# Optimization experiments

Measured on AMD Instinct MI355X. Metric: run time of the kernel, lower is better.

Reference implementation:

```python
import jax, jax.numpy as jnp
import numpy as np

N_NODES = 50000
N_EDGES = 600000
IN_CH, HID1, HID2, OUT_CH = 128, 256, 128, 2


def setup_inputs() -> dict:
    key = jax.random.key(0)
    ks = jax.random.split(key, 8)
    x = jax.random.normal(ks[0], (N_NODES, IN_CH), dtype=jnp.float32)
    edge_index = jax.random.randint(ks[1], (2, N_EDGES), 0, N_NODES, dtype=jnp.int64)
    # Glorot-style init for GCN linear weights
    def glorot(k, fan_in, fan_out):
        s = jnp.sqrt(6.0 / (fan_in + fan_out)).astype(jnp.float32)
        return jax.random.uniform(k, (fan_in, fan_out), jnp.float32, -s, s)
    return {
        "x": x,
        "W1": glorot(ks[2], IN_CH, HID1), "b1": jnp.zeros((HID1,), jnp.float32),
        "W2": glorot(ks[3], HID1, HID2), "b2": jnp.zeros((HID2,), jnp.float32),
        "W3": glorot(ks[4], HID2, OUT_CH), "b3": jnp.zeros((OUT_CH,), jnp.float32),
        "edge_index": edge_index,
    }


def _gcn_graph(edge_index, n_nodes):
    # Add self-loops (GCNConv default) and compute symmetric normalization
    loop = jnp.arange(n_nodes, dtype=edge_index.dtype)
    src = jnp.concatenate([edge_index[0], loop])
    dst = jnp.concatenate([edge_index[1], loop])
    ones = jnp.ones(src.shape[0], dtype=jnp.float32)
    deg = jax.ops.segment_sum(ones, dst, num_segments=n_nodes)
    dinv = jnp.where(deg > 0, jax.lax.rsqrt(deg), 0.0)
    norm = dinv[src] * dinv[dst]  # [E + N]
    return src, dst, norm


def _gcn_layer(h, W, b, src, dst, norm, n_nodes):
    h = h @ W                                   # [N, d_out]
    msg = h[src] * norm[:, None]                # gather + scale  [E+N, d_out]
    agg = jax.ops.segment_sum(msg, dst, num_segments=n_nodes)
    return agg + b


def reference(x, W1, b1, W2, b2, W3, b3, edge_index):
    n = x.shape[0]
    src, dst, norm = _gcn_graph(edge_index, n)
    h = jax.nn.relu(_gcn_layer(x, W1, b1, src, dst, norm, n))
    # dropout p=0.5 is identity in eval mode (training=False)
    h = jax.nn.relu(_gcn_layer(h, W2, b2, src, dst, norm, n))
    h = _gcn_layer(h, W3, b3, src, dst, norm, n)
    return jax.nn.log_softmax(h, axis=1)
```

## Files before the change

kernel.cpp:

```cpp
#include <hip/hip_runtime.h>
#include <hip/hip_bf16.h>
#include <math.h>

#define N_NODES 50000
#define N_EDGES 600000
#define E_TOT   (N_EDGES + N_NODES)
#define M_PAD   50048
#define NODE_STRIDE 32
#define DUMMY_ROWS 65536
#define CSR_CAP (N_NODES * NODE_STRIDE + 2048)

typedef __attribute__((ext_vector_type(8))) short bf16x8;
typedef __attribute__((ext_vector_type(4))) float f32x4;
typedef __attribute__((ext_vector_type(2))) float f32x2;
typedef __attribute__((ext_vector_type(8))) unsigned short u16x8;


__device__ __forceinline__ unsigned short f2bf(float f) {
    unsigned int u = __float_as_uint(f);
    unsigned int r = (u + 0x7fffu + ((u >> 16) & 1u)) >> 16;
    return (unsigned short)r;
}

__device__ __forceinline__ void acc_row(f32x2* acc, uint4 v) {
    acc[0] += (f32x2){__uint_as_float(v.x << 16), __uint_as_float(v.x & 0xffff0000u)};
    acc[1] += (f32x2){__uint_as_float(v.y << 16), __uint_as_float(v.y & 0xffff0000u)};
    acc[2] += (f32x2){__uint_as_float(v.z << 16), __uint_as_float(v.z & 0xffff0000u)};
    acc[3] += (f32x2){__uint_as_float(v.w << 16), __uint_as_float(v.w & 0xffff0000u)};
}

#define GLD_LDS16(g, l) __builtin_amdgcn_global_load_lds( \
    (__attribute__((address_space(1))) void*)(void*)(g), \
    (__attribute__((address_space(3))) void*)(l), 16, 0, 0)


__global__ void prep_kernel(const int* __restrict__ ei, int* __restrict__ cnt,
                            const float* __restrict__ W1, const float* __restrict__ W2,
                            unsigned short* __restrict__ W1t, unsigned short* __restrict__ W2t,
                            unsigned short* __restrict__ csr, unsigned short* __restrict__ xs,
                            unsigned short* __restrict__ t2b, float2* __restrict__ Ts) {
    const int NB_S = (E_TOT + 255) / 256;
    int b = blockIdx.x;
    if (b < NB_S) {
        int e = b * 256 + threadIdx.x;
        if (e >= E_TOT) return;
        int s, d;
        if (e < N_EDGES) { s = ei[e]; d = ei[N_EDGES + e]; }
        else             { s = d = e - N_EDGES; }
        int slot = atomicAdd(&cnt[d], 1);
        if (slot < NODE_STRIDE)
            csr[d * NODE_STRIDE + slot] = (unsigned short)s;
    } else if (b < NB_S + 128) {
        int i = (b - NB_S) * 256 + threadIdx.x;
        int k = i >> 8, n = i & 255;
        W1t[(size_t)n * 128 + k] = f2bf(W1[i]);
    } else if (b < NB_S + 256) {
        int i = (b - NB_S - 128) * 256 + threadIdx.x;
        int k = i >> 7, n = i & 127;
        W2t[(size_t)n * 256 + k] = f2bf(W2[i]);
    } else {
        int t = threadIdx.x;
        if (t < 16)
            *(uint4*)(xs + (size_t)(DUMMY_ROWS - 1) * 128 + t * 8) = make_uint4(0, 0, 0, 0);
        else if (t < 32)
            *(uint4*)(t2b + (size_t)(DUMMY_ROWS - 1) * 128 + (t - 16) * 8) = make_uint4(0, 0, 0, 0);
        else if (t == 32)
            Ts[DUMMY_ROWS - 1] = make_float2(0.f, 0.f);
    }
}


__global__ void scale_kernel(const int* __restrict__ cnt, const float* __restrict__ x,
                             unsigned short* __restrict__ xs, float* __restrict__ dinv) {
    const int NB_C = (N_NODES * 32 + 255) / 256;
    int b = blockIdx.x;
    if (b < NB_C) {
        int i = b * 256 + threadIdx.x;
        if (i >= N_NODES * 32) return;
        float d = rsqrtf((float)cnt[i >> 5]);
        float4 v = *(const float4*)(x + (size_t)i * 4);
        ushort4 o;
        o.x = f2bf(v.x * d); o.y = f2bf(v.y * d); o.z = f2bf(v.z * d); o.w = f2bf(v.w * d);
        *(ushort4*)(xs + (size_t)i * 4) = o;
    } else {
        int i = (b - NB_C) * 256 + threadIdx.x;
        if (i < N_NODES) dinv[i] = rsqrtf((float)cnt[i]);
    }
}


__global__ __launch_bounds__(256) void gemm12_kernel(
    const unsigned short* __restrict__ Hs,
    const float* __restrict__ dinv,
    const int* __restrict__ cnt,
    const unsigned short* __restrict__ csr,
    const unsigned short* __restrict__ W1t,
    const unsigned short* __restrict__ W2t,
    const float* __restrict__ b1,
    unsigned short* __restrict__ C,
    int M) {
    __shared__ __align__(16) unsigned short smem[64 * 256 + 64 * 128];
    unsigned short* Atile = smem;
    unsigned short* h1buf = smem;
    unsigned short* Bs    = smem + 64 * 256;
    int tid = threadIdx.x;
    int wave = tid >> 6, lane = tid & 63;
    int m0 = blockIdx.x * 64;
    int mm = lane & 15, kg = lane >> 4;
    int row0 = kg * 4;

    auto stage1 = [&](int n0) {
        #pragma unroll
        for (int it = 0; it < 4; ++it) {
            int ci = it * 256 + tid;
            int r = ci >> 4, c8 = (ci & 15) ^ (r & 15);
            const unsigned short* g = W1t + (size_t)(n0 + r) * 128 + c8 * 8;
            unsigned short* l = Bs + (size_t)(it * 256 + (tid & 192)) * 8;
            GLD_LDS16(g, l);
        }
    };
    auto stage2 = [&](int n0, int kh) {
        #pragma unroll
        for (int it = 0; it < 4; ++it) {
            int ci = it * 256 + tid;
            int r = ci >> 4, c8 = (ci & 15) ^ (r & 15);
            const unsigned short* g = W2t + (size_t)(n0 + r) * 256 + kh * 128 + c8 * 8;
            unsigned short* l = Bs + (size_t)(it * 256 + (tid & 192)) * 8;
            GLD_LDS16(g, l);
        }
    };

    stage1(0);

    {
        int q = tid & 15;
        int g = tid >> 4;
        #pragma unroll 1
        for (int nn = 0; nn < 4; ++nn) {
            int r = g * 4 + nn;
            int n = m0 + r;
            f32x2 acc2[4] = {};
            float dn = 0.f;
            if (n < M) {
                dn = dinv[n];
                int p = n * NODE_STRIDE;
                int pd = (cnt[n] + 3) & ~3;
                if (pd > NODE_STRIDE) pd = NODE_STRIDE;
                int pe = p + pd;
                ushort4 s4 = *(const ushort4*)(csr + p);
                while (p < pe) {
                    int pn = p + 4;
                    ushort4 nx = *(const ushort4*)(csr + pn);
                    uint4 v0 = *(const uint4*)(Hs + (size_t)s4.x * 128 + q * 8);
                    uint4 v1 = *(const uint4*)(Hs + (size_t)s4.y * 128 + q * 8);
                    uint4 v2 = *(const uint4*)(Hs + (size_t)s4.z * 128 + q * 8);
                    uint4 v3 = *(const uint4*)(Hs + (size_t)s4.w * 128 + q * 8);
                    acc_row(acc2, v0);
                    acc_row(acc2, v1);
                    acc_row(acc2, v2);
                    acc_row(acc2, v3);
                    p = pn; s4 = nx;
                }
            }
            float* acc = (float*)acc2;
            u16x8 ov;
            #pragma unroll
            for (int i2 = 0; i2 < 8; ++i2) ov[i2] = f2bf(acc[i2] * dn);
            *(u16x8*)(Atile + r * 128 + ((q ^ (r & 15)) * 8)) = ov;
        }
    }
    __syncthreads();

    bf16x8 aPre[4];
    #pragma unroll
    for (int kt = 0; kt < 4; ++kt) {
        int m = wave * 16 + mm;
        aPre[kt] = *(const bf16x8*)(Atile + m * 128 + (((kt * 4 + kg) ^ mm) * 8));
    }
    __syncthreads();

    int bb[4];
    #pragma unroll
    for (int j = 0; j < 4; ++j) bb[j] = (j * 16 + mm) * 128;
    int h1rd = (wave * 16 + mm) * 256;

    #pragma unroll 1
    for (int nt = 0; nt < 4; ++nt) {
        int n0 = nt * 64;
        f32x4 acc[4];
        #pragma unroll
        for (int j = 0; j < 4; ++j) acc[j] = (f32x4){0.f, 0.f, 0.f, 0.f};
        #pragma unroll
        for (int kt = 0; kt < 4; ++kt) {
            bf16x8 bfr[4];
            #pragma unroll
            for (int j = 0; j < 4; ++j)
                bfr[j] = *(const bf16x8*)(Bs + bb[j] + (((kt * 4 + kg) ^ mm) * 8));
            #pragma unroll
            for (int j = 0; j < 4; ++j)
                acc[j] = __builtin_amdgcn_mfma_f32_16x16x32_bf16(aPre[kt], bfr[j], acc[j], 0, 0, 0);
        }
        float bj[4];
        #pragma unroll
        for (int j = 0; j < 4; ++j) bj[j] = b1[n0 + j * 16 + mm];
        #pragma unroll
        for (int r = 0; r < 4; ++r) {
            int ml = wave * 16 + row0 + r;
            int rb = ml * 256, rx = ml & 15;
            #pragma unroll
            for (int j = 0; j < 4; ++j) {
                int c = n0 + j * 16 + mm;
                int c8 = c >> 3;
                float v = fmaxf(acc[j][r] + bj[j], 0.f);
                h1buf[rb + ((c8 ^ rx) * 8) + (c & 7)] = f2bf(v);
            }
        }
        __syncthreads();
        if (nt < 3) {
            stage1((nt + 1) * 64);
            __syncthreads();
        }
    }

    stage2(0, 0);
    #pragma unroll 1
    for (int nh = 0; nh < 2; ++nh) {
        int n0 = nh * 64;
        f32x4 acc[4];
        #pragma unroll
        for (int j = 0; j < 4; ++j) acc[j] = (f32x4){0.f, 0.f, 0.f, 0.f};
        #pragma unroll 1
        for (int kh = 0; kh < 2; ++kh) {
            __syncthreads();
            #pragma unroll
            for (int kt = 0; kt < 4; ++kt) {
                bf16x8 af, bfr[4];
                int c8h = kh * 16 + kt * 4 + kg;
                af = *(const bf16x8*)(h1buf + h1rd + ((c8h ^ mm) * 8));
                #pragma unroll
                for (int j = 0; j < 4; ++j)
                    bfr[j] = *(const bf16x8*)(Bs + bb[j] + (((kt * 4 + kg) ^ mm) * 8));
                #pragma unroll
                for (int j = 0; j < 4; ++j)
                    acc[j] = __builtin_amdgcn_mfma_f32_16x16x32_bf16(af, bfr[j], acc[j], 0, 0, 0);
            }
            __syncthreads();
            int s = nh * 2 + kh + 1;
            if (s < 4) stage2((s >> 1) * 64, s & 1);
        }
        #pragma unroll
        for (int r = 0; r < 4; ++r) {
            int gm = m0 + wave * 16 + row0 + r;
            float sc = (gm < M) ? dinv[gm] : 0.f;
            #pragma unroll
            for (int j = 0; j < 4; ++j) {
                int gn = n0 + j * 16 + mm;
                C[(size_t)gm * 128 + gn] = f2bf(acc[j][r] * sc);
            }
        }
    }
}


__global__ __launch_bounds__(256) void agg2_kernel(
    const unsigned short* __restrict__ Hs,
    const float* __restrict__ dinv,
    const int* __restrict__ cnt, const unsigned short* __restrict__ csr,
    const float* __restrict__ b2, const float* __restrict__ W3,
    float2* __restrict__ Ts) {
    int tid = threadIdx.x;
    int q = tid & 15;
    int g = tid >> 4;
    int n = blockIdx.x * 16 + g;
    if (n >= N_NODES) return;
    f32x2 acc2[4] = {};
    int p = n * NODE_STRIDE;
    int pd = (cnt[n] + 3) & ~3;
    if (pd > NODE_STRIDE) pd = NODE_STRIDE;
    int pe = p + pd;
    ushort4 s4 = *(const ushort4*)(csr + p);
    while (p < pe) {
        int pn = p + 4;
        ushort4 nx = *(const ushort4*)(csr + pn);
        uint4 v0 = *(const uint4*)(Hs + (size_t)s4.x * 128 + q * 8);
        uint4 v1 = *(const uint4*)(Hs + (size_t)s4.y * 128 + q * 8);
        uint4 v2 = *(const uint4*)(Hs + (size_t)s4.z * 128 + q * 8);
        uint4 v3 = *(const uint4*)(Hs + (size_t)s4.w * 128 + q * 8);
        acc_row(acc2, v0);
        acc_row(acc2, v1);
        acc_row(acc2, v2);
        acc_row(acc2, v3);
        p = pn; s4 = nx;
    }
    float dn = dinv[n];
    float* acc = (float*)acc2;
    float t0 = 0.f, t1 = 0.f;
    #pragma unroll
    for (int i = 0; i < 8; ++i) {
        int c = q * 8 + i;
        float h = fmaxf(acc[i] * dn + b2[c], 0.f);
        float2 w = ((const float2*)W3)[c];
        t0 += h * w.x; t1 += h * w.y;
    }
    #pragma unroll
    for (int off = 1; off < 16; off <<= 1) {
        t0 += __shfl_xor(t0, off);
        t1 += __shfl_xor(t1, off);
    }
    if (q == 0) Ts[n] = make_float2(t0 * dn, t1 * dn);
}


__global__ void lsm_kernel(const float2* __restrict__ Ts, const float* __restrict__ dinv,
                           const int* __restrict__ cnt, const unsigned short* __restrict__ csr,
                           const float* __restrict__ b3, float* __restrict__ out) {
    int n = blockIdx.x * 256 + threadIdx.x;
    if (n >= N_NODES) return;
    float a0 = 0.f, a1 = 0.f;
    int p0 = n * NODE_STRIDE;
    int pdeg = (cnt[n] + 3) & ~3;
    if (pdeg > NODE_STRIDE) pdeg = NODE_STRIDE;
    int pend = p0 + pdeg;
    ushort4 s4 = *(const ushort4*)(csr + p0);
    for (int p = p0; p < pend; p += 4) {
        ushort4 n4 = *(const ushort4*)(csr + p + 4);
        float2 u0 = Ts[s4.x], u1 = Ts[s4.y], u2 = Ts[s4.z], u3 = Ts[s4.w];
        a0 += (u0.x + u1.x) + (u2.x + u3.x);
        a1 += (u0.y + u1.y) + (u2.y + u3.y);
        s4 = n4;
    }
    float dn = dinv[n];
    float v0 = a0 * dn + b3[0];
    float v1 = a1 * dn + b3[1];
    float m = fmaxf(v0, v1);
    float lse = m + logf(expf(v0 - m) + expf(v1 - m));
    out[n * 2 + 0] = v0 - lse;
    out[n * 2 + 1] = v1 - lse;
}


extern "C" void kernel_launch(void* const* d_in, const int* in_sizes, int n_in,
                              void* d_out, int out_size, void* d_ws, size_t ws_size,
                              hipStream_t stream) {
    const float* x  = (const float*)d_in[0];
    const float* W1 = (const float*)d_in[1];
    const float* b1 = (const float*)d_in[2];
    const float* W2 = (const float*)d_in[3];
    const float* b2 = (const float*)d_in[4];
    const float* W3 = (const float*)d_in[5];
    const float* b3 = (const float*)d_in[6];
    const int*   ei = (const int*)d_in[7];
    float* out = (float*)d_out;

    char* ws = (char*)d_ws;
    size_t off = 0;
    auto alloc = [&](size_t bytes) -> char* {
        char* p = ws + off;
        off = (off + bytes + 255) & ~(size_t)255;
        return p;
    };
    int*   cnt  = (int*)alloc(N_NODES * 4);
    float* dinv = (float*)alloc(N_NODES * 4);
    unsigned short* csr = (unsigned short*)alloc((size_t)CSR_CAP * 2);
    unsigned short* xs     = (unsigned short*)alloc((size_t)DUMMY_ROWS * 128 * 2);
    unsigned short* W1t    = (unsigned short*)alloc((size_t)256 * 128 * 2);
    unsigned short* W2t    = (unsigned short*)alloc((size_t)128 * 256 * 2);
    unsigned short* t2b    = (unsigned short*)alloc((size_t)DUMMY_ROWS * 128 * 2);
    float2* Ts = (float2*)alloc((size_t)DUMMY_ROWS * 8);

    hipMemsetAsync(cnt, 0, N_NODES * 4, stream);
    hipMemsetAsync(csr, 0xFF, (size_t)CSR_CAP * 2, stream);

    const int NB_S = (E_TOT + 255) / 256;
    prep_kernel<<<NB_S + 256 + 1, 256, 0, stream>>>(
        ei, cnt, W1, W2, W1t, W2t, csr, xs, t2b, Ts);

    const int NB_C = (N_NODES * 32 + 255) / 256;
    const int NB_D = (N_NODES + 255) / 256;
    scale_kernel<<<NB_C + NB_D, 256, 0, stream>>>(cnt, x, xs, dinv);

    gemm12_kernel<<<M_PAD / 64, 256, 0, stream>>>(
        xs, dinv, cnt, csr, W1t, W2t, b1, t2b, N_NODES);
    agg2_kernel<<<(N_NODES + 15) / 16, 256, 0, stream>>>(
        t2b, dinv, cnt, csr, b2, W3, Ts);

    lsm_kernel<<<(N_NODES + 255) / 256, 256, 0, stream>>>(Ts, dinv, cnt, csr, b3, out);
}
```

Before: 203.8 us.

## Slice feature tables into 16-column slabs for cache-local gather aggregation

Stores the scaled input and layer-2 features as 8 column slices of 16 bf16 each, so every gather block touches only a 1.6 MB slice table and the random gathers stay in cache. Layer-1 aggregation is split out of the fused GEMM into its own sliced kernel that writes a sliced A matrix, which the GEMM then reads directly. Layer-2 aggregation is also sliced, and its partial W3 projections are combined with float atomics into a zeroed Ts buffer. In exchange it adds one extra kernel launch, an extra write and read of the aggregated layer-1 features, eightfold re-reading of the CSR indices, and atomic contention.

Result: slower. 223.0 us (+9.5%).

```diff
diff --git a/kernel.cpp b/kernel.cpp
--- a/kernel.cpp
+++ b/kernel.cpp
@@ -7,7 +7,8 @@
 #define E_TOT   (N_EDGES + N_NODES)
 #define M_PAD   50048
 #define NODE_STRIDE 32
-#define DUMMY_ROWS 65536
+#define TBL_PAD 65536
+#define N_SLICES 8
 #define CSR_CAP (N_NODES * NODE_STRIDE + 2048)
 
 typedef __attribute__((ext_vector_type(8))) short bf16x8;
@@ -37,8 +38,8 @@
 __global__ void prep_kernel(const int* __restrict__ ei, int* __restrict__ cnt,
                             const float* __restrict__ W1, const float* __restrict__ W2,
                             unsigned short* __restrict__ W1t, unsigned short* __restrict__ W2t,
-                            unsigned short* __restrict__ csr, unsigned short* __restrict__ xs,
-                            unsigned short* __restrict__ t2b, float2* __restrict__ Ts) {
+                            unsigned short* __restrict__ csr,
+                            unsigned short* __restrict__ xs_s, unsigned short* __restrict__ t2s) {
     const int NB_S = (E_TOT + 255) / 256;
     int b = blockIdx.x;
     if (b < NB_S) {
@@ -60,28 +61,35 @@
         W2t[(size_t)n * 256 + k] = f2bf(W2[i]);
     } else {
         int t = threadIdx.x;
-        if (t < 16)
-            *(uint4*)(xs + (size_t)(DUMMY_ROWS - 1) * 128 + t * 8) = make_uint4(0, 0, 0, 0);
-        else if (t < 32)
-            *(uint4*)(t2b + (size_t)(DUMMY_ROWS - 1) * 128 + (t - 16) * 8) = make_uint4(0, 0, 0, 0);
-        else if (t == 32)
-            Ts[DUMMY_ROWS - 1] = make_float2(0.f, 0.f);
+        if (t < 16) {
+            int sl = t >> 1, hf = t & 1;
+            *(uint4*)(xs_s + ((size_t)sl * TBL_PAD + (TBL_PAD - 1)) * 16 + hf * 8) =
+                make_uint4(0, 0, 0, 0);
+        } else if (t < 32) {
+            int u = t - 16;
+            int sl = u >> 1, hf = u & 1;
+            *(uint4*)(t2s + ((size_t)sl * TBL_PAD + (TBL_PAD - 1)) * 16 + hf * 8) =
+                make_uint4(0, 0, 0, 0);
+        }
     }
 }
 
 
 __global__ void scale_kernel(const int* __restrict__ cnt, const float* __restrict__ x,
-                             unsigned short* __restrict__ xs, float* __restrict__ dinv) {
+                             unsigned short* __restrict__ xs_s, float* __restrict__ dinv) {
     const int NB_C = (N_NODES * 32 + 255) / 256;
     int b = blockIdx.x;
     if (b < NB_C) {
         int i = b * 256 + threadIdx.x;
         if (i >= N_NODES * 32) return;
-        float d = rsqrtf((float)cnt[i >> 5]);
+        int node = i >> 5, cg = i & 31;
+        float d = rsqrtf((float)cnt[node]);
         float4 v = *(const float4*)(x + (size_t)i * 4);
         ushort4 o;
         o.x = f2bf(v.x * d); o.y = f2bf(v.y * d); o.z = f2bf(v.z * d); o.w = f2bf(v.w * d);
-        *(ushort4*)(xs + (size_t)i * 4) = o;
+        int sl = cg >> 2;
+        int wo = (cg & 3) * 4;
+        *(ushort4*)(xs_s + ((size_t)sl * TBL_PAD + node) * 16 + wo) = o;
     } else {
         int i = (b - NB_C) * 256 + threadIdx.x;
         if (i < N_NODES) dinv[i] = rsqrtf((float)cnt[i]);
@@ -89,20 +97,62 @@
 }
 
 
+__global__ __launch_bounds__(256) void agg1_kernel(
+    const unsigned short* __restrict__ xs_s, const float* __restrict__ dinv,
+    const int* __restrict__ cnt, const unsigned short* __restrict__ csr,
+    unsigned short* __restrict__ aggx_s) {
+    int slice = blockIdx.x & 7;
+    int node0 = (blockIdx.x >> 3) * 64;
+    int tid = threadIdx.x;
+    int g = tid >> 3, j = tid & 7;
+    int e = j >> 1, half = j & 1;
+    const unsigned short* tbl = xs_s + (size_t)slice * TBL_PAD * 16;
+    unsigned short* outb = aggx_s + (size_t)slice * M_PAD * 16;
+    #pragma unroll 1
+    for (int rnd = 0; rnd < 2; ++rnd) {
+        int n = node0 + rnd * 32 + g;
+        if (n >= M_PAD) continue;
+        f32x2 acc2[4] = {};
+        float dn = 0.f;
+        if (n < N_NODES) {
+            dn = dinv[n];
+            int p = n * NODE_STRIDE;
+            int pd = (cnt[n] + 3) & ~3;
+            if (pd > NODE_STRIDE) pd = NODE_STRIDE;
+            int pe = p + pd;
+            int idx = csr[p + e];
+            while (p < pe) {
+                int nx = csr[p + 4 + e];
+                uint4 v = *(const uint4*)(tbl + (size_t)idx * 16 + half * 8);
+                acc_row(acc2, v);
+                p += 4; idx = nx;
+            }
+        }
+        float* a = (float*)acc2;
+        #pragma unroll
+        for (int i = 0; i < 8; ++i) {
+            a[i] += __shfl_xor(a[i], 2);
+            a[i] += __shfl_xor(a[i], 4);
+        }
+        u16x8 ov;
+        #pragma unroll
+        for (int i = 0; i < 8; ++i) ov[i] = f2bf(a[i] * dn);
+        if (e == 0)
+            *(u16x8*)(outb + (size_t)n * 16 + half * 8) = ov;
+    }
+}
+
+
 __global__ __launch_bounds__(256) void gemm12_kernel(
-    const unsigned short* __restrict__ Hs,
-    const float* __restrict__ dinv,
-    const int* __restrict__ cnt,
-    const unsigned short* __restrict__ csr,
+    const unsigned short* __restrict__ A_s,
     const unsigned short* __restrict__ W1t,
     const unsigned short* __restrict__ W2t,
     const float* __restrict__ b1,
-    unsigned short* __restrict__ C,
+    const float* __restrict__ dinv,
+    unsigned short* __restrict__ t2s,
     int M) {
-    __shared__ __align__(16) unsigned short smem[64 * 256 + 64 * 128];
-    unsigned short* Atile = smem;
-    unsigned short* h1buf = smem;
-    unsigned short* Bs    = smem + 64 * 256;
+    __shared__ __align__(16) unsigned short h1buf[64 * 256];
+    __shared__ __align__(16) unsigned short Bs[64 * 128];
     int tid = threadIdx.x;
     int wave = tid >> 6, lane = tid & 63;
     int m0 = blockIdx.x * 64;
@@ -132,50 +182,12 @@
 
     stage1(0);
 
-    {
-        int q = tid & 15;
-        int g = tid >> 4;
-        #pragma unroll 1
-        for (int nn = 0; nn < 4; ++nn) {
-            int r = g * 4 + nn;
-            int n = m0 + r;
-            f32x2 acc2[4] = {};
-            float dn = 0.f;
-            if (n < M) {
-                dn = dinv[n];
-                int p = n * NODE_STRIDE;
-                int pd = (cnt[n] + 3) & ~3;
-                if (pd > NODE_STRIDE) pd = NODE_STRIDE;
-                int pe = p + pd;
-                ushort4 s4 = *(const ushort4*)(csr + p);
-                while (p < pe) {
-                    int pn = p + 4;
-                    ushort4 nx = *(const ushort4*)(csr + pn);
-                    uint4 v0 = *(const uint4*)(Hs + (size_t)s4.x * 128 + q * 8);
-                    uint4 v1 = *(const uint4*)(Hs + (size_t)s4.y * 128 + q * 8);
-                    uint4 v2 = *(const uint4*)(Hs + (size_t)s4.z * 128 + q * 8);
-                    uint4 v3 = *(const uint4*)(Hs + (size_t)s4.w * 128 + q * 8);
-                    acc_row(acc2, v0);
-                    acc_row(acc2, v1);
-                    acc_row(acc2, v2);
-                    acc_row(acc2, v3);
-                    p = pn; s4 = nx;
-                }
-            }
-            float* acc = (float*)acc2;
-            u16x8 ov;
-            #pragma unroll
-            for (int i2 = 0; i2 < 8; ++i2) ov[i2] = f2bf(acc[i2] * dn);
-            *(u16x8*)(Atile + r * 128 + ((q ^ (r & 15)) * 8)) = ov;
-        }
-    }
-    __syncthreads();
-
     bf16x8 aPre[4];
     #pragma unroll
     for (int kt = 0; kt < 4; ++kt) {
-        int m = wave * 16 + mm;
-        aPre[kt] = *(const bf16x8*)(Atile + m * 128 + (((kt * 4 + kg) ^ mm) * 8));
+        int c0 = kt * 32 + kg * 8;
+        aPre[kt] = *(const bf16x8*)(A_s + ((size_t)(c0 >> 4) * M_PAD + m0 + wave * 16 + mm) * 16
+                                    + (c0 & 8));
     }
     __syncthreads();
 
@@ -255,7 +267,8 @@
             #pragma unroll
             for (int j = 0; j < 4; ++j) {
                 int gn = n0 + j * 16 + mm;
-                C[(size_t)gm * 128 + gn] = f2bf(acc[j][r] * sc);
+                int sl = gn >> 4;
+                t2s[((size_t)sl * TBL_PAD + gm) * 16 + (gn & 15)] = f2bf(acc[j][r] * sc);
             }
         }
     }
@@ -263,51 +276,55 @@
 
 
 __global__ __launch_bounds__(256) void agg2_kernel(
-    const unsigned short* __restrict__ Hs,
-    const float* __restrict__ dinv,
+    const unsigned short* __restrict__ t2s, const float* __restrict__ dinv,
     const int* __restrict__ cnt, const unsigned short* __restrict__ csr,
     const float* __restrict__ b2, const float* __restrict__ W3,
     float2* __restrict__ Ts) {
+    int slice = blockIdx.x & 7;
+    int node0 = (blockIdx.x >> 3) * 64;
     int tid = threadIdx.x;
-    int q = tid & 15;
-    int g = tid >> 4;
-    int n = blockIdx.x * 16 + g;
-    if (n >= N_NODES) return;
-    f32x2 acc2[4] = {};
-    int p = n * NODE_STRIDE;
-    int pd = (cnt[n] + 3) & ~3;
-    if (pd > NODE_STRIDE) pd = NODE_STRIDE;
-    int pe = p + pd;
-    ushort4 s4 = *(const ushort4*)(csr + p);
-    while (p < pe) {
-        int pn = p + 4;
-        ushort4 nx = *(const ushort4*)(csr + pn);
-        uint4 v0 = *(const uint4*)(Hs + (size_t)s4.x * 128 + q * 8);
-        uint4 v1 = *(const uint4*)(Hs + (size_t)s4.y * 128 + q * 8);
-        uint4 v2 = *(const uint4*)(Hs + (size_t)s4.z * 128 + q * 8);
-        uint4 v3 = *(const uint4*)(Hs + (size_t)s4.w * 128 + q * 8);
-        acc_row(acc2, v0);
-        acc_row(acc2, v1);
-        acc_row(acc2, v2);
-        acc_row(acc2, v3);
-        p = pn; s4 = nx;
-    }
-    float dn = dinv[n];
-    float* acc = (float*)acc2;
-    float t0 = 0.f, t1 = 0.f;
-    #pragma unroll
-    for (int i = 0; i < 8; ++i) {
-        int c = q * 8 + i;
-        float h = fmaxf(acc[i] * dn + b2[c], 0.f);
-        float2 w = ((const float2*)W3)[c];
-        t0 += h * w.x; t1 += h * w.y;
-    }
-    #pragma unroll
-    for (int off = 1; off < 16; off <<= 1) {
-        t0 += __shfl_xor(t0, off);
-        t1 += __shfl_xor(t1, off);
-    }
-    if (q == 0) Ts[n] = make_float2(t0 * dn, t1 * dn);
+    int g = tid >> 3, j = tid & 7;
+    int e = j >> 1, half = j & 1;
+    const unsigned short* tbl = t2s + (size_t)slice * TBL_PAD * 16;
+    #pragma unroll 1
+    for (int rnd = 0; rnd < 2; ++rnd) {
+        int n = node0 + rnd * 32 + g;
+        if (n >= N_NODES) continue;
+        f32x2 acc2[4] = {};
+        float dn = dinv[n];
+        int p = n * NODE_STRIDE;
+        int pd = (cnt[n] + 3) & ~3;
+        if (pd > NODE_STRIDE) pd = NODE_STRIDE;
+        int pe = p + pd;
+        int idx = csr[p + e];
+        while (p < pe) {
+            int nx = csr[p + 4 + e];
+            uint4 v = *(const uint4*)(tbl + (size_t)idx * 16 + half * 8);
+            acc_row(acc2, v);
+            p += 4; idx = nx;
+        }
+        float* a = (float*)acc2;
+        #pragma unroll
+        for (int i = 0; i < 8; ++i) {
+            a[i] += __shfl_xor(a[i], 2);
+            a[i] += __shfl_xor(a[i], 4);
+        }
+        float t0 = 0.f, t1 = 0.f;
+        int c0 = slice * 16 + half * 8;
+        #pragma unroll
+        for (int i = 0; i < 8; ++i) {
+            int c = c0 + i;
+            float h = fmaxf(a[i] * dn + b2[c], 0.f);
+            float2 w = ((const float2*)W3)[c];
+            t0 += h * w.x; t1 += h * w.y;
+        }
+        t0 += __shfl_xor(t0, 1);
+        t1 += __shfl_xor(t1, 1);
+        if (j == 0) {
+            atomicAdd((float*)(Ts + n), t0 * dn);
+            atomicAdd((float*)(Ts + n) + 1, t1 * dn);
+        }
+    }
 }
 
 
@@ -362,27 +379,31 @@
     int*   cnt  = (int*)alloc(N_NODES * 4);
     float* dinv = (float*)alloc(N_NODES * 4);
     unsigned short* csr = (unsigned short*)alloc((size_t)CSR_CAP * 2);
-    unsigned short* xs     = (unsigned short*)alloc((size_t)DUMMY_ROWS * 128 * 2);
+    unsigned short* xs_s   = (unsigned short*)alloc((size_t)N_SLICES * TBL_PAD * 16 * 2);
     unsigned short* W1t    = (unsigned short*)alloc((size_t)256 * 128 * 2);
     unsigned short* W2t    = (unsigned short*)alloc((size_t)128 * 256 * 2);
-    unsigned short* t2b    = (unsigned short*)alloc((size_t)DUMMY_ROWS * 128 * 2);
-    float2* Ts = (float2*)alloc((size_t)DUMMY_ROWS * 8);
+    unsigned short* aggx_s = (unsigned short*)alloc((size_t)N_SLICES * M_PAD * 16 * 2);
+    unsigned short* t2s    = (unsigned short*)alloc((size_t)N_SLICES * TBL_PAD * 16 * 2);
+    float2* Ts = (float2*)alloc((size_t)TBL_PAD * 8);
 
     hipMemsetAsync(cnt, 0, N_NODES * 4, stream);
     hipMemsetAsync(csr, 0xFF, (size_t)CSR_CAP * 2, stream);
+    hipMemsetAsync(Ts, 0, (size_t)TBL_PAD * 8, stream);
 
     const int NB_S = (E_TOT + 255) / 256;
     prep_kernel<<<NB_S + 256 + 1, 256, 0, stream>>>(
-        ei, cnt, W1, W2, W1t, W2t, csr, xs, t2b, Ts);
+        ei, cnt, W1, W2, W1t, W2t, csr, xs_s, t2s);
 
     const int NB_C = (N_NODES * 32 + 255) / 256;
     const int NB_D = (N_NODES + 255) / 256;
-    scale_kernel<<<NB_C + NB_D, 256, 0, stream>>>(cnt, x, xs, dinv);
-
+    scale_kernel<<<NB_C + NB_D, 256, 0, stream>>>(cnt, x, xs_s, dinv);
+
+    agg1_kernel<<<N_SLICES * (M_PAD / 64), 256, 0, stream>>>(
+        xs_s, dinv, cnt, csr, aggx_s);
     gemm12_kernel<<<M_PAD / 64, 256, 0, stream>>>(
-        xs, dinv, cnt, csr, W1t, W2t, b1, t2b, N_NODES);
-    agg2_kernel<<<(N_NODES + 15) / 16, 256, 0, stream>>>(
-        t2b, dinv, cnt, csr, b2, W3, Ts);
+        aggx_s, W1t, W2t, b1, dinv, t2s, N_NODES);
+    agg2_kernel<<<N_SLICES * (M_PAD / 64), 256, 0, stream>>>(
+        t2s, dinv, cnt, csr, b2, W3, Ts);
 
     lsm_kernel<<<(N_NODES + 255) / 256, 256, 0, stream>>>(Ts, dinv, cnt, csr, b3, out);
 }
```

## Split layer-1 aggregation into wave-per-node kernel and edge-split both gathers

Applied to the files above, without the earlier changes.

The layer-1 neighbour aggregation moves out of the fused GEMM kernel into a new agg1 kernel. In it, one 64-lane wave handles one node: four quarter-waves each take a strided share of the edge list, then combine their partial sums with cross-lane shuffles. The aggregated bf16 rows go to a new global buffer that the GEMM kernel loads its A fragments from directly. agg2 gets the same wave-per-node, edge-split layout. This aims to expose more memory-level parallelism in the gather phase. The cost is an extra launch, a global write and read of the aggregated features, and more padded dummy-row gathers, since degrees are now rounded up to 16.

Result: no change. 201.5 us (-1.1%).

```diff
diff --git a/kernel.cpp b/kernel.cpp
--- a/kernel.cpp
+++ b/kernel.cpp
@@ -89,20 +89,62 @@
 }
 
 
+__global__ __launch_bounds__(256) void agg1_kernel(
+    const unsigned short* __restrict__ Hs, const float* __restrict__ dinv,
+    const int* __restrict__ cnt, const unsigned short* __restrict__ csr,
+    unsigned short* __restrict__ outb) {
+    int wave = threadIdx.x >> 6;
+    int lane = threadIdx.x & 63;
+    int n = blockIdx.x * 4 + wave;
+    if (n >= N_NODES) return;
+    int quarter = lane >> 4;
+    int q = lane & 15;
+    f32x2 acc2[4] = {};
+    int p0 = n * NODE_STRIDE;
+    int pdeg = (cnt[n] + 15) & ~15;
+    if (pdeg > NODE_STRIDE) pdeg = NODE_STRIDE;
+    int pend = p0 + pdeg;
+    int p = p0 + quarter * 4;
+    ushort4 s4 = *(const ushort4*)(csr + p);
+    while (p < pend) {
+        int pn = p + 16;
+        ushort4 n4 = *(const ushort4*)(csr + pn);
+        uint4 v0 = *(const uint4*)(Hs + (size_t)s4.x * 128 + q * 8);
+        uint4 v1 = *(const uint4*)(Hs + (size_t)s4.y * 128 + q * 8);
+        uint4 v2 = *(const uint4*)(Hs + (size_t)s4.z * 128 + q * 8);
+        uint4 v3 = *(const uint4*)(Hs + (size_t)s4.w * 128 + q * 8);
+        acc_row(acc2, v0);
+        acc_row(acc2, v1);
+        acc_row(acc2, v2);
+        acc_row(acc2, v3);
+        p = pn; s4 = n4;
+    }
+    float* acc = (float*)acc2;
+    #pragma unroll
+    for (int i = 0; i < 8; ++i) {
+        acc[i] += __shfl_xor(acc[i], 16);
+        acc[i] += __shfl_xor(acc[i], 32);
+    }
+    float dn = dinv[n];
+    if (quarter == 0) {
+        u16x8 ov;
+        #pragma unroll
+        for (int i = 0; i < 8; ++i) ov[i] = f2bf(acc[i] * dn);
+        *(u16x8*)(outb + (size_t)n * 128 + q * 8) = ov;
+    }
+}
+
+
 __global__ __launch_bounds__(256) void gemm12_kernel(
-    const unsigned short* __restrict__ Hs,
-    const float* __restrict__ dinv,
-    const int* __restrict__ cnt,
-    const unsigned short* __restrict__ csr,
+    const unsigned short* __restrict__ A,
     const unsigned short* __restrict__ W1t,
     const unsigned short* __restrict__ W2t,
     const float* __restrict__ b1,
+    const float* __restrict__ dinv,
     unsigned short* __restrict__ C,
     int M) {
-    __shared__ __align__(16) unsigned short smem[64 * 256 + 64 * 128];
-    unsigned short* Atile = smem;
-    unsigned short* h1buf = smem;
-    unsigned short* Bs    = smem + 64 * 256;
+    __shared__ __align__(16) unsigned short h1buf[64 * 256];
+    __shared__ __align__(16) unsigned short Bs[64 * 128];
     int tid = threadIdx.x;
     int wave = tid >> 6, lane = tid & 63;
     int m0 = blockIdx.x * 64;
@@ -132,50 +174,11 @@
 
     stage1(0);
 
-    {
-        int q = tid & 15;
-        int g = tid >> 4;
-        #pragma unroll 1
-        for (int nn = 0; nn < 4; ++nn) {
-            int r = g * 4 + nn;
-            int n = m0 + r;
-            f32x2 acc2[4] = {};
-            float dn = 0.f;
-            if (n < M) {
-                dn = dinv[n];
-                int p = n * NODE_STRIDE;
-                int pd = (cnt[n] + 3) & ~3;
-                if (pd > NODE_STRIDE) pd = NODE_STRIDE;
-                int pe = p + pd;
-                ushort4 s4 = *(const ushort4*)(csr + p);
-                while (p < pe) {
-                    int pn = p + 4;
-                    ushort4 nx = *(const ushort4*)(csr + pn);
-                    uint4 v0 = *(const uint4*)(Hs + (size_t)s4.x * 128 + q * 8);
-                    uint4 v1 = *(const uint4*)(Hs + (size_t)s4.y * 128 + q * 8);
-                    uint4 v2 = *(const uint4*)(Hs + (size_t)s4.z * 128 + q * 8);
-                    uint4 v3 = *(const uint4*)(Hs + (size_t)s4.w * 128 + q * 8);
-                    acc_row(acc2, v0);
-                    acc_row(acc2, v1);
-                    acc_row(acc2, v2);
-                    acc_row(acc2, v3);
-                    p = pn; s4 = nx;
-                }
-            }
-            float* acc = (float*)acc2;
-            u16x8 ov;
-            #pragma unroll
-            for (int i2 = 0; i2 < 8; ++i2) ov[i2] = f2bf(acc[i2] * dn);
-            *(u16x8*)(Atile + r * 128 + ((q ^ (r & 15)) * 8)) = ov;
-        }
-    }
-    __syncthreads();
-
     bf16x8 aPre[4];
     #pragma unroll
     for (int kt = 0; kt < 4; ++kt) {
-        int m = wave * 16 + mm;
-        aPre[kt] = *(const bf16x8*)(Atile + m * 128 + (((kt * 4 + kg) ^ mm) * 8));
+        int m = m0 + wave * 16 + mm;
+        aPre[kt] = *(const bf16x8*)(A + (size_t)m * 128 + kt * 32 + kg * 8);
     }
     __syncthreads();
 
@@ -268,20 +271,22 @@
     const int* __restrict__ cnt, const unsigned short* __restrict__ csr,
     const float* __restrict__ b2, const float* __restrict__ W3,
     float2* __restrict__ Ts) {
-    int tid = threadIdx.x;
-    int q = tid & 15;
-    int g = tid >> 4;
-    int n = blockIdx.x * 16 + g;
+    int wave = threadIdx.x >> 6;
+    int lane = threadIdx.x & 63;
+    int n = blockIdx.x * 4 + wave;
     if (n >= N_NODES) return;
+    int quarter = lane >> 4;
+    int q = lane & 15;
     f32x2 acc2[4] = {};
-    int p = n * NODE_STRIDE;
-    int pd = (cnt[n] + 3) & ~3;
-    if (pd > NODE_STRIDE) pd = NODE_STRIDE;
-    int pe = p + pd;
+    int p0 = n * NODE_STRIDE;
+    int pdeg = (cnt[n] + 15) & ~15;
+    if (pdeg > NODE_STRIDE) pdeg = NODE_STRIDE;
+    int pend = p0 + pdeg;
+    int p = p0 + quarter * 4;
     ushort4 s4 = *(const ushort4*)(csr + p);
-    while (p < pe) {
-        int pn = p + 4;
-        ushort4 nx = *(const ushort4*)(csr + pn);
+    while (p < pend) {
+        int pn = p + 16;
+        ushort4 n4 = *(const ushort4*)(csr + pn);
         uint4 v0 = *(const uint4*)(Hs + (size_t)s4.x * 128 + q * 8);
         uint4 v1 = *(const uint4*)(Hs + (size_t)s4.y * 128 + q * 8);
         uint4 v2 = *(const uint4*)(Hs + (size_t)s4.z * 128 + q * 8);
@@ -290,10 +295,15 @@
         acc_row(acc2, v1);
         acc_row(acc2, v2);
         acc_row(acc2, v3);
-        p = pn; s4 = nx;
+        p = pn; s4 = n4;
+    }
+    float* acc = (float*)acc2;
+    #pragma unroll
+    for (int i = 0; i < 8; ++i) {
+        acc[i] += __shfl_xor(acc[i], 16);
+        acc[i] += __shfl_xor(acc[i], 32);
     }
     float dn = dinv[n];
-    float* acc = (float*)acc2;
     float t0 = 0.f, t1 = 0.f;
     #pragma unroll
     for (int i = 0; i < 8; ++i) {
@@ -307,7 +317,7 @@
         t0 += __shfl_xor(t0, off);
         t1 += __shfl_xor(t1, off);
     }
-    if (q == 0) Ts[n] = make_float2(t0 * dn, t1 * dn);
+    if (lane == 0) Ts[n] = make_float2(t0 * dn, t1 * dn);
 }
 
 
@@ -365,6 +375,7 @@
     unsigned short* xs     = (unsigned short*)alloc((size_t)DUMMY_ROWS * 128 * 2);
     unsigned short* W1t    = (unsigned short*)alloc((size_t)256 * 128 * 2);
     unsigned short* W2t    = (unsigned short*)alloc((size_t)128 * 256 * 2);
+    unsigned short* aggx   = (unsigned short*)alloc((size_t)M_PAD * 128 * 2);
     unsigned short* t2b    = (unsigned short*)alloc((size_t)DUMMY_ROWS * 128 * 2);
     float2* Ts = (float2*)alloc((size_t)DUMMY_ROWS * 8);
 
@@ -379,9 +390,11 @@
     const int NB_D = (N_NODES + 255) / 256;
     scale_kernel<<<NB_C + NB_D, 256, 0, stream>>>(cnt, x, xs, dinv);
 
+    agg1_kernel<<<(N_NODES + 3) / 4, 256, 0, stream>>>(
+        xs, dinv, cnt, csr, aggx);
     gemm12_kernel<<<M_PAD / 64, 256, 0, stream>>>(
-        xs, dinv, cnt, csr, W1t, W2t, b1, t2b, N_NODES);
-    agg2_kernel<<<(N_NODES + 15) / 16, 256, 0, stream>>>(
+        aggx, W1t, W2t, b1, dinv, t2b, N_NODES);
+    agg2_kernel<<<(N_NODES + 3) / 4, 256, 0, stream>>>(
         t2b, dinv, cnt, csr, b2, W3, Ts);
 
     lsm_kernel<<<(N_NODES + 255) / 256, 256, 0, stream>>>(Ts, dinv, cnt, csr, b3, out);
```

## Widen fused GCN block to 512 threads, split agg2 edges across wave quarters

Applied to the files above, without the earlier changes.

The fused aggregate+GEMM kernel now runs 512 threads per block, so each wave computes half the output columns and the gather phase handles 32 rows per pass. agg2 assigns one wave per node, with its four 16-lane quarters taking interleaved edge chunks and combining partial sums through shuffles. The full CSR 0xFF memset is dropped; scale_kernel instead fills only the unused padding slots per node. These aim to raise parallelism on the gather, cut memset traffic, and improve latency hiding, at the cost of more syncs per thread and extra shuffle reductions.

Result: faster. 198.8 us (-2.4%).

```diff
diff --git a/kernel.cpp b/kernel.cpp
--- a/kernel.cpp
+++ b/kernel.cpp
@@ -71,7 +71,8 @@
 
 
 __global__ void scale_kernel(const int* __restrict__ cnt, const float* __restrict__ x,
-                             unsigned short* __restrict__ xs, float* __restrict__ dinv) {
+                             unsigned short* __restrict__ xs, float* __restrict__ dinv,
+                             unsigned short* __restrict__ csr) {
     const int NB_C = (N_NODES * 32 + 255) / 256;
     int b = blockIdx.x;
     if (b < NB_C) {
@@ -84,12 +85,18 @@
         *(ushort4*)(xs + (size_t)i * 4) = o;
     } else {
         int i = (b - NB_C) * 256 + threadIdx.x;
-        if (i < N_NODES) dinv[i] = rsqrtf((float)cnt[i]);
-    }
-}
-
-
-__global__ __launch_bounds__(256) void gemm12_kernel(
+        if (i < N_NODES) {
+            int c = cnt[i];
+            dinv[i] = rsqrtf((float)c);
+            if (c > NODE_STRIDE) c = NODE_STRIDE;
+            for (int s = c; s < NODE_STRIDE; ++s)
+                csr[i * NODE_STRIDE + s] = 0xFFFFu;
+        }
+    }
+}
+
+
+__global__ __launch_bounds__(512, 6) void fused1_kernel(
     const unsigned short* __restrict__ Hs,
     const float* __restrict__ dinv,
     const int* __restrict__ cnt,
@@ -104,28 +111,29 @@
     unsigned short* h1buf = smem;
     unsigned short* Bs    = smem + 64 * 256;
     int tid = threadIdx.x;
-    int wave = tid >> 6, lane = tid & 63;
+    int lane = tid & 63;
     int m0 = blockIdx.x * 64;
     int mm = lane & 15, kg = lane >> 4;
-    int row0 = kg * 4;
+    int rowg = (tid >> 6) & 3;
+    int colg = tid >> 8;
 
     auto stage1 = [&](int n0) {
         #pragma unroll
-        for (int it = 0; it < 4; ++it) {
-            int ci = it * 256 + tid;
+        for (int it = 0; it < 2; ++it) {
+            int ci = it * 512 + tid;
             int r = ci >> 4, c8 = (ci & 15) ^ (r & 15);
             const unsigned short* g = W1t + (size_t)(n0 + r) * 128 + c8 * 8;
-            unsigned short* l = Bs + (size_t)(it * 256 + (tid & 192)) * 8;
+            unsigned short* l = Bs + (size_t)(it * 512 + (tid & 448)) * 8;
             GLD_LDS16(g, l);
         }
     };
     auto stage2 = [&](int n0, int kh) {
         #pragma unroll
-        for (int it = 0; it < 4; ++it) {
-            int ci = it * 256 + tid;
+        for (int it = 0; it < 2; ++it) {
+            int ci = it * 512 + tid;
             int r = ci >> 4, c8 = (ci & 15) ^ (r & 15);
             const unsigned short* g = W2t + (size_t)(n0 + r) * 256 + kh * 128 + c8 * 8;
-            unsigned short* l = Bs + (size_t)(it * 256 + (tid & 192)) * 8;
+            unsigned short* l = Bs + (size_t)(it * 512 + (tid & 448)) * 8;
             GLD_LDS16(g, l);
         }
     };
@@ -136,12 +144,12 @@
         int q = tid & 15;
         int g = tid >> 4;
         #pragma unroll 1
-        for (int nn = 0; nn < 4; ++nn) {
-            int r = g * 4 + nn;
+        for (int pass = 0; pass < 2; ++pass) {
+            int r = pass * 32 + g;
             int n = m0 + r;
             f32x2 acc2[4] = {};
             float dn = 0.f;
-            if (n < M) {
+            if (n < N_NODES) {
                 dn = dinv[n];
                 int p = n * NODE_STRIDE;
                 int pd = (cnt[n] + 3) & ~3;
@@ -174,42 +182,42 @@
     bf16x8 aPre[4];
     #pragma unroll
     for (int kt = 0; kt < 4; ++kt) {
-        int m = wave * 16 + mm;
-        aPre[kt] = *(const bf16x8*)(Atile + m * 128 + (((kt * 4 + kg) ^ mm) * 8));
+        int ml = rowg * 16 + mm;
+        aPre[kt] = *(const bf16x8*)(Atile + ml * 128 + (((kt * 4 + kg) ^ mm) * 8));
     }
     __syncthreads();
 
-    int bb[4];
+    int bb[2];
     #pragma unroll
-    for (int j = 0; j < 4; ++j) bb[j] = (j * 16 + mm) * 128;
-    int h1rd = (wave * 16 + mm) * 256;
+    for (int j = 0; j < 2; ++j) bb[j] = (colg * 32 + j * 16 + mm) * 128;
+    int h1rd = (rowg * 16 + mm) * 256;
 
     #pragma unroll 1
     for (int nt = 0; nt < 4; ++nt) {
         int n0 = nt * 64;
-        f32x4 acc[4];
-        #pragma unroll
-        for (int j = 0; j < 4; ++j) acc[j] = (f32x4){0.f, 0.f, 0.f, 0.f};
+        f32x4 acc[2];
+        #pragma unroll
+        for (int j = 0; j < 2; ++j) acc[j] = (f32x4){0.f, 0.f, 0.f, 0.f};
         #pragma unroll
         for (int kt = 0; kt < 4; ++kt) {
-            bf16x8 bfr[4];
-            #pragma unroll
-            for (int j = 0; j < 4; ++j)
+            bf16x8 bfr[2];
+            #pragma unroll
+            for (int j = 0; j < 2; ++j)
                 bfr[j] = *(const bf16x8*)(Bs + bb[j] + (((kt * 4 + kg) ^ mm) * 8));
             #pragma unroll
-            for (int j = 0; j < 4; ++j)
+            for (int j = 0; j < 2; ++j)
                 acc[j] = __builtin_amdgcn_mfma_f32_16x16x32_bf16(aPre[kt], bfr[j], acc[j], 0, 0, 0);
         }
-        float bj[4];
-        #pragma unroll
-        for (int j = 0; j < 4; ++j) bj[j] = b1[n0 + j * 16 + mm];
+        float bj[2];
+        #pragma unroll
+        for (int j = 0; j < 2; ++j) bj[j] = b1[n0 + colg * 32 + j * 16 + mm];
         #pragma unroll
         for (int r = 0; r < 4; ++r) {
-            int ml = wave * 16 + row0 + r;
+            int ml = rowg * 16 + kg * 4 + r;
             int rb = ml * 256, rx = ml & 15;
             #pragma unroll
-            for (int j = 0; j < 4; ++j) {
-                int c = n0 + j * 16 + mm;
+            for (int j = 0; j < 2; ++j) {
+                int c = n0 + colg * 32 + j * 16 + mm;
                 int c8 = c >> 3;
                 float v = fmaxf(acc[j][r] + bj[j], 0.f);
                 h1buf[rb + ((c8 ^ rx) * 8) + (c & 7)] = f2bf(v);
@@ -226,22 +234,22 @@
     #pragma unroll 1
     for (int nh = 0; nh < 2; ++nh) {
         int n0 = nh * 64;
-        f32x4 acc[4];
-        #pragma unroll
-        for (int j = 0; j < 4; ++j) acc[j] = (f32x4){0.f, 0.f, 0.f, 0.f};
+        f32x4 acc[2];
+        #pragma unroll
+        for (int j = 0; j < 2; ++j) acc[j] = (f32x4){0.f, 0.f, 0.f, 0.f};
         #pragma unroll 1
         for (int kh = 0; kh < 2; ++kh) {
             __syncthreads();
             #pragma unroll
             for (int kt = 0; kt < 4; ++kt) {
-                bf16x8 af, bfr[4];
+                bf16x8 af, bfr[2];
                 int c8h = kh * 16 + kt * 4 + kg;
                 af = *(const bf16x8*)(h1buf + h1rd + ((c8h ^ mm) * 8));
                 #pragma unroll
-                for (int j = 0; j < 4; ++j)
+                for (int j = 0; j < 2; ++j)
                     bfr[j] = *(const bf16x8*)(Bs + bb[j] + (((kt * 4 + kg) ^ mm) * 8));
                 #pragma unroll
-                for (int j = 0; j < 4; ++j)
+                for (int j = 0; j < 2; ++j)
                     acc[j] = __builtin_amdgcn_mfma_f32_16x16x32_bf16(af, bfr[j], acc[j], 0, 0, 0);
             }
             __syncthreads();
@@ -250,11 +258,11 @@
         }
         #pragma unroll
         for (int r = 0; r < 4; ++r) {
-            int gm = m0 + wave * 16 + row0 + r;
+            int gm = m0 + rowg * 16 + kg * 4 + r;
             float sc = (gm < M) ? dinv[gm] : 0.f;
             #pragma unroll
-            for (int j = 0; j < 4; ++j) {
-                int gn = n0 + j * 16 + mm;
+            for (int j = 0; j < 2; ++j) {
+                int gn = nh * 64 + colg * 32 + j * 16 + mm;
                 C[(size_t)gm * 128 + gn] = f2bf(acc[j][r] * sc);
             }
         }
@@ -268,20 +276,22 @@
     const int* __restrict__ cnt, const unsigned short* __restrict__ csr,
     const float* __restrict__ b2, const float* __restrict__ W3,
     float2* __restrict__ Ts) {
-    int tid = threadIdx.x;
-    int q = tid & 15;
-    int g = tid >> 4;
-    int n = blockIdx.x * 16 + g;
+    int wave = threadIdx.x >> 6;
+    int lane = threadIdx.x & 63;
+    int n = blockIdx.x * 4 + wave;
     if (n >= N_NODES) return;
+    int quarter = lane >> 4;
+    int q = lane & 15;
     f32x2 acc2[4] = {};
-    int p = n * NODE_STRIDE;
-    int pd = (cnt[n] + 3) & ~3;
-    if (pd > NODE_STRIDE) pd = NODE_STRIDE;
-    int pe = p + pd;
+    int p0 = n * NODE_STRIDE;
+    int pdeg = (cnt[n] + 15) & ~15;
+    if (pdeg > NODE_STRIDE) pdeg = NODE_STRIDE;
+    int pend = p0 + pdeg;
+    int p = p0 + quarter * 4;
     ushort4 s4 = *(const ushort4*)(csr + p);
-    while (p < pe) {
-        int pn = p + 4;
-        ushort4 nx = *(const ushort4*)(csr + pn);
+    while (p < pend) {
+        int pn = p + 16;
+        ushort4 n4 = *(const ushort4*)(csr + pn);
         uint4 v0 = *(const uint4*)(Hs + (size_t)s4.x * 128 + q * 8);
         uint4 v1 = *(const uint4*)(Hs + (size_t)s4.y * 128 + q * 8);
         uint4 v2 = *(const uint4*)(Hs + (size_t)s4.z * 128 + q * 8);
@@ -290,10 +300,15 @@
         acc_row(acc2, v1);
         acc_row(acc2, v2);
         acc_row(acc2, v3);
-        p = pn; s4 = nx;
+        p = pn; s4 = n4;
+    }
+    float* acc = (float*)acc2;
+    #pragma unroll
+    for (int i = 0; i < 8; ++i) {
+        acc[i] += __shfl_xor(acc[i], 16);
+        acc[i] += __shfl_xor(acc[i], 32);
     }
     float dn = dinv[n];
-    float* acc = (float*)acc2;
     float t0 = 0.f, t1 = 0.f;
     #pragma unroll
     for (int i = 0; i < 8; ++i) {
@@ -307,7 +322,7 @@
         t0 += __shfl_xor(t0, off);
         t1 += __shfl_xor(t1, off);
     }
-    if (q == 0) Ts[n] = make_float2(t0 * dn, t1 * dn);
+    if (lane == 0) Ts[n] = make_float2(t0 * dn, t1 * dn);
 }
 
 
@@ -369,7 +384,6 @@
     float2* Ts = (float2*)alloc((size_t)DUMMY_ROWS * 8);
 
     hipMemsetAsync(cnt, 0, N_NODES * 4, stream);
-    hipMemsetAsync(csr, 0xFF, (size_t)CSR_CAP * 2, stream);
 
     const int NB_S = (E_TOT + 255) / 256;
     prep_kernel<<<NB_S + 256 + 1, 256, 0, stream>>>(
@@ -377,11 +391,11 @@
 
     const int NB_C = (N_NODES * 32 + 255) / 256;
     const int NB_D = (N_NODES + 255) / 256;
-    scale_kernel<<<NB_C + NB_D, 256, 0, stream>>>(cnt, x, xs, dinv);
-
-    gemm12_kernel<<<M_PAD / 64, 256, 0, stream>>>(
+    scale_kernel<<<NB_C + NB_D, 256, 0, stream>>>(cnt, x, xs, dinv, csr);
+
+    fused1_kernel<<<M_PAD / 64, 512, 0, stream>>>(
         xs, dinv, cnt, csr, W1t, W2t, b1, t2b, N_NODES);
-    agg2_kernel<<<(N_NODES + 15) / 16, 256, 0, stream>>>(
+    agg2_kernel<<<(N_NODES + 3) / 4, 256, 0, stream>>>(
         t2b, dinv, cnt, csr, b2, W3, Ts);
 
     lsm_kernel<<<(N_NODES + 255) / 256, 256, 0, stream>>>(Ts, dinv, cnt, csr, b3, out);
```
